# Kernel tuning notes

Measured on AMD Instinct MI355X. Metric: run time of the kernel, lower is better.

The kernel has to match this reference:

```python
import jax, jax.numpy as jnp
import numpy as np

KH, KW, PAD = 32, 32, 10  # kernel_size and padding from NeuralMem.__init__


def setup_inputs() -> dict:
    key = jax.random.key(0)
    k1, k2, k3, k4 = jax.random.split(key, 4)
    image = jax.random.normal(k1, (64, 64, 3), dtype=jnp.float32)
    mem = jax.random.normal(k2, (8192, 3072), dtype=jnp.float32)    # faiss IndexFlatL2 bank (keys)
    mem2 = jax.random.normal(k3, (8192, 3072), dtype=jnp.float32)   # faiss reconstruction bank (values)
    mapping = jax.random.randint(k4, (8192,), 0, 8192)              # Counter.most_common(1) vote table
    return {"image": image, "mem": mem, "mem2": mem2, "mapping": mapping}


def reference(image, mem, mem2, mapping):
    H, W, C = image.shape
    x = image.transpose(2, 0, 1)                       # [C,H,W]  (permute(2,0,1))
    xp = jnp.pad(x, ((0, 0), (PAD, PAD), (PAD, PAD)))  # unfold padding
    Lh = H + 2 * PAD - KH + 1
    Lw = W + 2 * PAD - KW + 1
    ii = jnp.arange(Lh)[:, None] + jnp.arange(KH)[None, :]  # [Lh,KH]
    jj = jnp.arange(Lw)[:, None] + jnp.arange(KW)[None, :]  # [Lw,KW]
    # unfold: patches [C,Lh,KH,Lw,KW] -> [L, C*KH*KW] with torch's (C,kh,kw) column order
    patches = xp[:, ii[:, :, None, None], jj[None, None, :, :]]
    patches = patches.transpose(1, 3, 0, 2, 4).reshape(Lh * Lw, C * KH * KW)  # [L,D]
    # L2 kNN (k=1): argmin ||p - m||^2 = argmin (||m||^2 - 2 p.m); ||p||^2 is constant per row
    mem_sq = jnp.sum(mem * mem, axis=1)                # [N]
    scores = patches @ mem.T                           # [L,N]
    nn = jnp.argmin(mem_sq[None, :] - 2.0 * scores, axis=1)  # [L]
    # counter majority vote -> mem2 reconstruct
    recon = mem2[mapping[nn]]                          # [L,D]
    # fold (sum of overlapping patches), then crop padding
    rp = recon.reshape(Lh, Lw, C, KH, KW).transpose(2, 0, 3, 1, 4)  # [C,Lh,KH,Lw,KW]
    outp = jnp.zeros_like(xp).at[:, ii[:, :, None, None], jj[None, None, :, :]].add(rp)
    out = outp[:, PAD:PAD + H, PAD:PAD + W]            # [C,H,W]
    out = out / jnp.max(out)                           # out / out.flatten().max()
    return out.transpose(1, 2, 0)                      # [H,W,C]
```

## Files before the change

### kernel.cpp

```cpp
#include <hip/hip_runtime.h>

typedef unsigned short u16;
typedef unsigned int   u32;
typedef int      i32x4  __attribute__((ext_vector_type(4)));
typedef float    f32x4  __attribute__((ext_vector_type(4)));
typedef _Float16 f16x8  __attribute__((ext_vector_type(8)));

#define LHW   53
#define NP    2809
#define KDIM  3072
#define NMEM  8192
#define PADW  84
#define IMG   64
#define MPAD  2816
#define BIGF  3.402823466e+38f
#define MARGIN 24.0f
#define QS    31.75f
#define C2    (2.0f / (QS * QS))

#define O_XP    0UL
#define O_MSQ   84736UL
#define O_MI8   117504UL
#define O_AI8   25283328UL
#define O_D     33934080UL
#define O_PVAL  80071424UL
#define O_ROWI  81524480UL
#define O_ACC   81535744UL
#define WS_NEED5 81584896UL

#define F_XP    0
#define F_MSQ   21504
#define F_PVAL  29696
#define F_PIDX  119584
#define F_ROW   209472
#define F_ACC   212288
#define F_MAX   224576
#define NSPL    32
#define NRANGE  (NMEM / NSPL)

__device__ inline char q8(float x) {
    float y = x * QS;
    y = fminf(fmaxf(y, -127.f), 127.f);
    return (char)__float2int_rn(y);
}

__global__ void k_xp(const float* __restrict__ image, float* __restrict__ xp,
                     float* __restrict__ accb) {
    int id = blockIdx.x * 256 + threadIdx.x;
    if (id < 12288) accb[id] = 0.f;
    if (id < 3 * PADW * PADW) {
        int c = id / (PADW * PADW), rem = id % (PADW * PADW);
        int py = rem / PADW, px = rem % PADW;
        float v = 0.f;
        if (py >= 10 && py < 74 && px >= 10 && px < 74)
            v = image[((py - 10) * IMG + (px - 10)) * 3 + c];
        xp[id] = v;
    }
}

__global__ __launch_bounds__(1024) void k_maxnorm(const float* __restrict__ acc,
                                                  float* __restrict__ out) {
    int t = threadIdx.x;
    float m = -BIGF;
    for (int i = t; i < 12288; i += 1024) m = fmaxf(m, acc[i]);
    #pragma unroll
    for (int s = 1; s < 64; s <<= 1) m = fmaxf(m, __shfl_xor(m, s));
    __shared__ float ls[16];
    int lane = t & 63, w = t >> 6;
    if (lane == 0) ls[w] = m;
    __syncthreads();
    float mv = ls[0];
    #pragma unroll
    for (int i = 1; i < 16; ++i) mv = fmaxf(mv, ls[i]);
    for (int i = t; i < 12288; i += 1024) {
        int c = i >> 12, y = (i >> 6) & 63, x = i & 63;
        out[(y * IMG + x) * 3 + c] = acc[i] / mv;
    }
}

__global__ __launch_bounds__(256) void k_quantmsq(const float* __restrict__ mem,
                                                  char* __restrict__ mq,
                                                  float* __restrict__ msq) {
    int j = blockIdx.x, t = threadIdx.x;
    const float4* r4 = (const float4*)(mem + (size_t)j * KDIM);
    char4* q4 = (char4*)(mq + (size_t)j * KDIM);
    float s = 0.f;
    #pragma unroll
    for (int i = 0; i < 3; ++i) {
        int idx = i * 256 + t;
        float4 v = r4[idx];
        s += v.x * v.x + v.y * v.y + v.z * v.z + v.w * v.w;
        char4 q = {q8(v.x), q8(v.y), q8(v.z), q8(v.w)};
        q4[idx] = q;
    }
    #pragma unroll
    for (int m = 1; m < 64; m <<= 1) s += __shfl_xor(s, m);
    __shared__ float ls[4];
    int lane = t & 63, w = t >> 6;
    if (lane == 0) ls[w] = s;
    __syncthreads();
    if (t == 0) msq[j] = ls[0] + ls[1] + ls[2] + ls[3];
}

__global__ __launch_bounds__(256) void k_quant_A(const float* __restrict__ xp,
                                                 char* __restrict__ aq) {
    int id = blockIdx.x * 256 + threadIdx.x;
    int e0 = id * 4;
    int p = e0 / KDIM, k = e0 - p * KDIM;
    char4 q = {0, 0, 0, 0};
    if (p < NP) {
        int c = k >> 10, kh = (k >> 5) & 31, kw = k & 31;
        int lh = p / LHW, lw = p - lh * LHW;
        const float* src = xp + c * (PADW * PADW) + (lh + kh) * PADW + lw + kw;
        q.x = q8(src[0]); q.y = q8(src[1]); q.z = q8(src[2]); q.w = q8(src[3]);
    }
    ((char4*)aq)[id] = q;
}

__global__ __launch_bounds__(256) void k_gemm_i8(
    const char* __restrict__ Aq, const char* __restrict__ Bq,
    const float* __restrict__ msq, _Float16* __restrict__ Dm,
    float* __restrict__ pval)
{
    __shared__ __align__(16) char lds[65536];
    const int t = threadIdx.x;
    const int lane = t & 63;
    const int w = t >> 6, wm = w >> 1, wn = w & 1;
    const int mrow = lane & 15;

    int L = blockIdx.x;
    int logical = (L & 7) * 176 + (L >> 3);
    int by = logical / 22, bx = logical - by * 22;
    const int rowBase = bx * 128;
    const int jBase   = by * 128;

    const int lrow = lane >> 3;
    const int gsrc = (lane & 7) ^ lrow;
    const char* gpl[8];
    unsigned ldsb[8];
    #pragma unroll
    for (int s = 0; s < 8; ++s) {
        int P = s >> 2, sub = s & 3;
        int row = sub * 32 + w * 8 + lrow;
        const char* basep = (P == 0 ? Aq : Bq);
        int gRow = (P == 0 ? rowBase : jBase) + row;
        gpl[s]  = basep + (size_t)gRow * KDIM + gsrc * 16;
        ldsb[s] = P * 16384 + (unsigned)(sub * 32 + w * 8) * 128;
    }

    i32x4 acc[4][4];
    #pragma unroll
    for (int i = 0; i < 4; ++i)
        #pragma unroll
        for (int j = 0; j < 4; ++j) { i32x4 z = {0, 0, 0, 0}; acc[i][j] = z; }

    #pragma unroll
    for (int s = 0; s < 8; ++s)
        __builtin_amdgcn_global_load_lds(
            (const __attribute__((address_space(1))) void*)(gpl[s]),
            (__attribute__((address_space(3))) void*)(lds + ldsb[s]),
            16, 0, 0);

    for (int kc = 0; kc < 24; ++kc) {
        const int cb = kc & 1;
        __syncthreads();
        if (kc < 23) {
            const unsigned nb = (cb ^ 1) * 32768u;
            #pragma unroll
            for (int s = 0; s < 8; ++s)
                __builtin_amdgcn_global_load_lds(
                    (const __attribute__((address_space(1))) void*)(gpl[s] + (kc + 1) * 128),
                    (__attribute__((address_space(3))) void*)(lds + nb + ldsb[s]),
                    16, 0, 0);
        }
        const char* lbase = lds + cb * 32768;
        #pragma unroll
        for (int kh2 = 0; kh2 < 2; ++kh2) {
            const int grp = kh2 * 4 + (lane >> 4);
            i32x4 ah[4];
            #pragma unroll
            for (int f = 0; f < 4; ++f) {
                int ra = wm * 64 + f * 16 + mrow;
                ah[f] = *(const i32x4*)(lbase + ra * 128 + (grp ^ (ra & 7)) * 16);
            }
            #pragma unroll
            for (int fj = 0; fj < 4; ++fj) {
                int rb = wn * 64 + fj * 16 + mrow;
                i32x4 bh = *(const i32x4*)(lbase + 16384 + rb * 128 + (grp ^ (rb & 7)) * 16);
                #pragma unroll
                for (int fi = 0; fi < 4; ++fi)
                    acc[fi][fj] = __builtin_amdgcn_mfma_i32_16x16x64_i8(ah[fi], bh, acc[fi][fj], 0, 0, 0);
            }
        }
    }

    float ms[4];
    #pragma unroll
    for (int fj = 0; fj < 4; ++fj) ms[fj] = msq[jBase + wn * 64 + fj * 16 + mrow] - 3072.0f;
    const int splitId = by * 2 + wn;
    #pragma unroll
    for (int fi = 0; fi < 4; ++fi) {
        #pragma unroll
        for (int r = 0; r < 4; ++r) {
            int p = rowBase + wm * 64 + fi * 16 + (lane >> 4) * 4 + r;
            float bv = BIGF;
            #pragma unroll
            for (int fj = 0; fj < 4; ++fj) {
                int j = jBase + wn * 64 + fj * 16 + mrow;
                float d = fmaf(-C2, (float)acc[fi][fj][r], ms[fj]);
                Dm[(size_t)p * NMEM + j] = (_Float16)d;
                bv = fminf(bv, d);
            }
            #pragma unroll
            for (int m = 1; m < 16; m <<= 1) bv = fminf(bv, __shfl_xor(bv, m));
            if (mrow == 0 && p < NP)
                pval[(size_t)p * 128 + splitId] = bv;
        }
    }
}

__global__ __launch_bounds__(256) void k_refine(
    const _Float16* __restrict__ Dm, const float* __restrict__ pval,
    const float* __restrict__ msq, const float* __restrict__ xp,
    const float* __restrict__ mem, const int* __restrict__ mapping,
    int* __restrict__ rowIdx)
{
    const int p = blockIdx.x, t = threadIdx.x;
    const _Float16* row = Dm + (size_t)p * NMEM;
    const int lane = t & 63, w = t >> 6;

    __shared__ float wred[4];
    __shared__ int lcnt;
    __shared__ int list[256];
    __shared__ float thr_s;

    float pm = (t < 128) ? pval[(size_t)p * 128 + t] : BIGF;
    #pragma unroll
    for (int m = 1; m < 64; m <<= 1) pm = fminf(pm, __shfl_xor(pm, m));
    if (lane == 0) wred[w] = pm;
    if (t == 0) lcnt = 0;
    __syncthreads();
    if (t == 0)
        thr_s = fminf(fminf(wred[0], wred[1]), fminf(wred[2], wred[3]))
                + (MARGIN + 0.5f);
    __syncthreads();
    const float th = thr_s;

    #pragma unroll
    for (int i0 = 0; i0 < 4; ++i0) {
        int base = i0 * 2048 + t * 8;
        f16x8 v = *(const f16x8*)(row + base);
        #pragma unroll
        for (int e = 0; e < 8; ++e)
            if ((float)v[e] <= th) {
                int sl = atomicAdd(&lcnt, 1);
                if (sl < 256) list[sl] = base + e;
            }
    }
    __syncthreads();
    int nc = min(lcnt, 256);

    const int lh = p / LHW, lw = p - (p / LHW) * LHW;
    float bd = BIGF; int bj = 0x7fffffff;
    __shared__ float tot;
    for (int ci = 0; ci < nc; ++ci) {
        int j = list[ci];
        const float* mrow2 = mem + (size_t)j * KDIM;
        float s = 0.f;
        for (int k = t; k < KDIM; k += 256) {
            int c = k >> 10, kh = (k >> 5) & 31, kw = k & 31;
            s += xp[c * (PADW * PADW) + (lh + kh) * PADW + lw + kw] * mrow2[k];
        }
        #pragma unroll
        for (int m = 1; m < 64; m <<= 1) s += __shfl_xor(s, m);
        if (lane == 0) wred[w] = s;
        __syncthreads();
        if (t == 0) tot = wred[0] + wred[1] + wred[2] + wred[3];
        __syncthreads();
        float d = msq[j] - 2.f * tot;
        if (d < bd || (d == bd && j < bj)) { bd = d; bj = j; }
    }
    if (t == 0) rowIdx[p] = mapping[bj];
}

#define LWCH 4
__global__ __launch_bounds__(256) void k_scatter(const float* __restrict__ mem2,
                                                 const int* __restrict__ rowIdx,
                                                 float* __restrict__ accb) {
    int b = blockIdx.x;
    int ch = b & (LWCH - 1);
    int lc = b >> 2;
    const int lh = lc / 3, c = lc % 3;
    const int lw0 = ch * 14, lw1 = min(53, lw0 + 14);
    __shared__ int r2s[53];
    const int t = threadIdx.x;
    if (t >= lw0 && t < lw1) r2s[t] = rowIdx[lh * LHW + t];
    __syncthreads();
    const int kh = t >> 3;
    const int g  = t & 7;
    float s[11];
    #pragma unroll
    for (int u = 0; u < 11; ++u) s[u] = 0.f;
    for (int lw = lw0; lw < lw1; ++lw) {
        const float* rowp = mem2 + (size_t)r2s[lw] * KDIM + c * 1024 + kh * 32;
        #pragma unroll
        for (int u = 0; u < 11; ++u) {
            int kw = g + 8 * u - lw;
            if (kw >= 0 && kw < 32) s[u] += rowp[kw];
        }
    }
    const int y = lh + kh - 10;
    if (y >= 0 && y < 64) {
        #pragma unroll
        for (int u = 0; u < 11; ++u) {
            int x = g + 8 * u - 10;
            if (x >= 0 && x < 64 && s[u] != 0.f)
                atomicAdd(&accb[c * 4096 + y * 64 + x], s[u]);
        }
    }
}

__global__ __launch_bounds__(256) void k_msq(const float* __restrict__ mem,
                                             float* __restrict__ msq) {
    int j = blockIdx.x;
    const float* row = mem + (size_t)j * KDIM;
    float s = 0.f;
    for (int i = threadIdx.x; i < KDIM; i += 256) { float v = row[i]; s += v * v; }
    #pragma unroll
    for (int m = 1; m < 64; m <<= 1) s += __shfl_xor(s, m);
    __shared__ float ls[4];
    int lane = threadIdx.x & 63, w = threadIdx.x >> 6;
    if (lane == 0) ls[w] = s;
    __syncthreads();
    if (threadIdx.x == 0) msq[j] = ls[0] + ls[1] + ls[2] + ls[3];
}

__global__ void k_amin(const float* __restrict__ pval, const int* __restrict__ pidx,
                       const int* __restrict__ mapping, int* __restrict__ rowIdx,
                       int nspl) {
    int p = blockIdx.x * 256 + threadIdx.x;
    if (p < NP) {
        float bv = BIGF; int bi = 0x7fffffff;
        for (int ns = 0; ns < nspl; ++ns) {
            float v = pval[(size_t)p * nspl + ns];
            int ix = pidx[(size_t)p * nspl + ns];
            if (v < bv || (v == bv && ix < bi)) { bv = v; bi = ix; }
        }
        rowIdx[p] = mapping[bi];
    }
}

__global__ __launch_bounds__(256) void k_gather(const float* __restrict__ mem2,
                                                const int* __restrict__ rowIdx,
                                                float* __restrict__ acc) {
    int b = blockIdx.x;
    int c = b >> 12, y = (b >> 6) & 63, x = b & 63;
    int khmin = max(0, y - 42), khmax = min(31, y + 10);
    int kwmin = max(0, x - 42), kwmax = min(31, x + 10);
    int nh = khmax - khmin + 1, nw = kwmax - kwmin + 1;
    int total = nh * nw;
    float s = 0.f;
    for (int idx = threadIdx.x; idx < total; idx += 256) {
        int kh = khmin + idx / nw;
        int kw = kwmin + idx % nw;
        int lh = y + 10 - kh, lw = x + 10 - kw;
        int p = lh * LHW + lw;
        int r2 = rowIdx[p];
        s += mem2[(size_t)r2 * KDIM + c * 1024 + kh * 32 + kw];
    }
    #pragma unroll
    for (int m = 1; m < 64; m <<= 1) s += __shfl_xor(s, m);
    __shared__ float ls[4];
    int lane = threadIdx.x & 63, w = threadIdx.x >> 6;
    if (lane == 0) ls[w] = s;
    __syncthreads();
    if (threadIdx.x == 0) acc[b] = ls[0] + ls[1] + ls[2] + ls[3];
}

__global__ __launch_bounds__(256) void k_gemm_argmin(
    const float* __restrict__ xp, const float* __restrict__ mem,
    const float* __restrict__ msq, float* __restrict__ pval,
    int* __restrict__ pidx)
{
    __shared__ float At[64][33];
    __shared__ float Bt[64][33];
    const int t = threadIdx.x;
    const int tx = t & 15, ty = t >> 4;
    const int rowBase = blockIdx.x * 64;
    const int nBase = blockIdx.y * NRANGE;

    float best[4]; int bidx[4];
    #pragma unroll
    for (int i = 0; i < 4; ++i) { best[i] = BIGF; bidx[i] = 0x7fffffff; }

    for (int nt = 0; nt < NRANGE / 64; ++nt) {
        const int jBase = nBase + nt * 64;
        float acc[4][4];
        #pragma unroll
        for (int i = 0; i < 4; ++i)
            #pragma unroll
            for (int j = 0; j < 4; ++j) acc[i][j] = 0.f;

        for (int kc = 0; kc < KDIM / 32; ++kc) {
            const int c = kc >> 5, kh = kc & 31;
            const float* xpc = xp + c * (PADW * PADW) + kh * PADW;
            #pragma unroll
            for (int i = 0; i < 8; ++i) {
                int e = i * 256 + t;
                int r = e >> 5, kwi = e & 31;
                int p = rowBase + r;
                float v = 0.f;
                if (p < NP) {
                    int lh = p / LHW, lw = p - lh * LHW;
                    v = xpc[lh * PADW + lw + kwi];
                }
                At[r][kwi] = v;
            }
            const float* mb = mem + (size_t)jBase * KDIM + kc * 32;
            #pragma unroll
            for (int i = 0; i < 8; ++i) {
                int e = i * 256 + t;
                int r = e >> 5, kwi = e & 31;
                Bt[r][kwi] = mb[(size_t)r * KDIM + kwi];
            }
            __syncthreads();
            #pragma unroll
            for (int kk = 0; kk < 32; ++kk) {
                float a[4], b[4];
                #pragma unroll
                for (int i = 0; i < 4; ++i) a[i] = At[ty + 16 * i][kk];
                #pragma unroll
                for (int j = 0; j < 4; ++j) b[j] = Bt[tx + 16 * j][kk];
                #pragma unroll
                for (int i = 0; i < 4; ++i)
                    #pragma unroll
                    for (int j = 0; j < 4; ++j) acc[i][j] += a[i] * b[j];
            }
            __syncthreads();
        }
        #pragma unroll
        for (int j = 0; j < 4; ++j) {
            int col = jBase + tx + 16 * j;
            float msv = msq[col];
            #pragma unroll
            for (int i = 0; i < 4; ++i) {
                float d = msv - 2.f * acc[i][j];
                if (d < best[i] || (d == best[i] && col < bidx[i])) {
                    best[i] = d; bidx[i] = col;
                }
            }
        }
    }
    #pragma unroll
    for (int m = 1; m < 16; m <<= 1) {
        #pragma unroll
        for (int i = 0; i < 4; ++i) {
            float ov = __shfl_xor(best[i], m);
            int   oi = __shfl_xor(bidx[i], m);
            if (ov < best[i] || (ov == best[i] && oi < bidx[i])) {
                best[i] = ov; bidx[i] = oi;
            }
        }
    }
    if (tx == 0) {
        #pragma unroll
        for (int i = 0; i < 4; ++i) {
            int p = rowBase + ty + 16 * i;
            if (p < NP) {
                pval[p * NSPL + blockIdx.y] = best[i];
                pidx[p * NSPL + blockIdx.y] = bidx[i];
            }
        }
    }
}

__global__ __launch_bounds__(256) void k_max(const float* __restrict__ acc,
                                             float* __restrict__ maxv) {
    float m = -BIGF;
    for (int i = threadIdx.x; i < 12288; i += 256) m = fmaxf(m, acc[i]);
    #pragma unroll
    for (int s = 1; s < 64; s <<= 1) m = fmaxf(m, __shfl_xor(m, s));
    __shared__ float ls[4];
    int lane = threadIdx.x & 63, w = threadIdx.x >> 6;
    if (lane == 0) ls[w] = m;
    __syncthreads();
    if (threadIdx.x == 0)
        maxv[0] = fmaxf(fmaxf(ls[0], ls[1]), fmaxf(ls[2], ls[3]));
}

__global__ void k_norm(const float* __restrict__ acc, const float* __restrict__ maxv,
                       float* __restrict__ out) {
    int id = blockIdx.x * 256 + threadIdx.x;
    if (id < 12288) {
        int c = id >> 12, y = (id >> 6) & 63, x = id & 63;
        out[(y * IMG + x) * 3 + c] = acc[id] / maxv[0];
    }
}

extern "C" void kernel_launch(void* const* d_in, const int* in_sizes, int n_in,
                              void* d_out, int out_size, void* d_ws, size_t ws_size,
                              hipStream_t stream) {
    const float* image   = (const float*)d_in[0];
    const float* mem     = (const float*)d_in[1];
    const float* mem2    = (const float*)d_in[2];
    const int*   mapping = (const int*)d_in[3];

    if (ws_size >= WS_NEED5) {
        char* wsB = (char*)d_ws;
        float*    xp   = (float*)(wsB + O_XP);
        float*    msq  = (float*)(wsB + O_MSQ);
        char*     mI8  = (char*)(wsB + O_MI8);
        char*     aI8  = (char*)(wsB + O_AI8);
        _Float16* Dm   = (_Float16*)(wsB + O_D);
        float*    pval = (float*)(wsB + O_PVAL);
        int*      rowI = (int*)(wsB + O_ROWI);
        float*    accb = (float*)(wsB + O_ACC);

        k_xp<<<dim3((3 * PADW * PADW + 255) / 256), 256, 0, stream>>>(image, xp, accb);
        k_quantmsq<<<dim3(NMEM), 256, 0, stream>>>(mem, mI8, msq);
        k_quant_A<<<dim3(MPAD * KDIM / 4 / 256), 256, 0, stream>>>(xp, aI8);
        k_gemm_i8<<<dim3(1408), 256, 0, stream>>>(aI8, mI8, msq, Dm, pval);
        k_refine<<<dim3(NP), 256, 0, stream>>>(Dm, pval, msq, xp, mem, mapping, rowI);
        k_scatter<<<dim3(LHW * 3 * LWCH), 256, 0, stream>>>(mem2, rowI, accb);
        k_maxnorm<<<dim3(1), 1024, 0, stream>>>(accb, (float*)d_out);
    } else {
        float* ws   = (float*)d_ws;
        float* xp   = ws + F_XP;
        float* msq  = ws + F_MSQ;
        float* pval = ws + F_PVAL;
        int*   pidx = (int*)(ws + F_PIDX);
        int*   rowI = (int*)(ws + F_ROW);
        float* acc  = ws + F_ACC;
        float* maxv = ws + F_MAX;

        k_xp<<<dim3((3 * PADW * PADW + 255) / 256), 256, 0, stream>>>(image, xp, acc);
        k_msq<<<dim3(NMEM), 256, 0, stream>>>(mem, msq);
        k_gemm_argmin<<<dim3((NP + 63) / 64, NSPL), 256, 0, stream>>>(xp, mem, msq, pval, pidx);
        k_amin<<<dim3((NP + 255) / 256), 256, 0, stream>>>(pval, pidx, mapping, rowI, NSPL);
        k_gather<<<dim3(3 * IMG * IMG), 256, 0, stream>>>(mem2, rowI, acc);
        k_max<<<dim3(1), 256, 0, stream>>>(acc, maxv);
        k_norm<<<dim3((12288 + 255) / 256), 256, 0, stream>>>(acc, maxv, (float*)d_out);
    }
}
```

Measured before the change: 202.2 us.

## Switch coarse kNN screening GEMM from int8 to FP4 scaled MFMA

Quantizes both the memory bank and the image patches to packed 4-bit E2M1 values instead of int8. The screening GEMM then uses the scaled f8f6f4 MFMA in FP4 mode, which halves the bytes loaded per row and the number of K iterations. The goal is to cut the cost of the coarse distance GEMM and of the quantization passes. Because FP4 is much coarser, the refine threshold margin grows from 24 to 128. That admits more candidates into exact refinement and risks dropping the true nearest neighbour if more than the capped 256 candidates fall inside the threshold.

```diff
diff --git a/kernel.cpp b/kernel.cpp
--- a/kernel.cpp
+++ b/kernel.cpp
@@ -3,6 +3,7 @@
 typedef unsigned short u16;
 typedef unsigned int   u32;
 typedef int      i32x4  __attribute__((ext_vector_type(4)));
+typedef int      i32x8  __attribute__((ext_vector_type(8)));
 typedef float    f32x4  __attribute__((ext_vector_type(4)));
 typedef _Float16 f16x8  __attribute__((ext_vector_type(8)));
 
@@ -14,19 +15,18 @@
 #define IMG   64
 #define MPAD  2816
 #define BIGF  3.402823466e+38f
-#define MARGIN 24.0f
-#define QS    31.75f
-#define C2    (2.0f / (QS * QS))
+#define MARGIN 128.0f
+#define ROWB  1536
 
 #define O_XP    0UL
 #define O_MSQ   84736UL
-#define O_MI8   117504UL
-#define O_AI8   25283328UL
-#define O_D     33934080UL
-#define O_PVAL  80071424UL
-#define O_ROWI  81524480UL
-#define O_ACC   81535744UL
-#define WS_NEED5 81584896UL
+#define O_MQ4   117504UL
+#define O_AQ4   12700416UL
+#define O_D     17025792UL
+#define O_PVAL  63163136UL
+#define O_ROWI  64604928UL
+#define O_ACC   64616192UL
+#define WS_NEED6 64665344UL
 
 #define F_XP    0
 #define F_MSQ   21504
@@ -38,10 +38,20 @@
 #define NSPL    32
 #define NRANGE  (NMEM / NSPL)
 
-__device__ inline char q8(float x) {
-    float y = x * QS;
-    y = fminf(fmaxf(y, -127.f), 127.f);
-    return (char)__float2int_rn(y);
+__device__ inline u32 q4(float x) {
+    float a = fminf(fabsf(x), 6.0f);
+    u32 s = (__float_as_uint(x) >> 31) << 3;
+    int v2;
+    if (a < 2.0f)      v2 = __float2int_rn(a * 2.0f);
+    else if (a < 4.0f) v2 = __float2int_rn(a) * 2;
+    else               v2 = __float2int_rn(a * 0.5f) * 4;
+    u32 e;
+    if (v2 <= 3)      e = (u32)v2;
+    else if (v2 == 4) e = 4u;
+    else if (v2 == 6) e = 5u;
+    else if (v2 == 8) e = 6u;
+    else              e = 7u;
+    return s | e;
 }
 
 __global__ void k_xp(const float* __restrict__ image, float* __restrict__ xp,
@@ -78,20 +88,19 @@
     }
 }
 
-__global__ __launch_bounds__(256) void k_quantmsq(const float* __restrict__ mem,
-                                                  char* __restrict__ mq,
-                                                  float* __restrict__ msq) {
+__global__ __launch_bounds__(256) void k_quantmsq4(const float* __restrict__ mem,
+                                                   u16* __restrict__ mq,
+                                                   float* __restrict__ msq) {
     int j = blockIdx.x, t = threadIdx.x;
-    const float4* r4 = (const float4*)(mem + (size_t)j * KDIM);
-    char4* q4 = (char4*)(mq + (size_t)j * KDIM);
+    const float4* r4 = (const float4*)(mem + (size_t)j * KDIM + t * 12);
+    u16* dst = mq + (size_t)j * (ROWB / 2) + t * 3;
     float s = 0.f;
     #pragma unroll
-    for (int i = 0; i < 3; ++i) {
-        int idx = i * 256 + t;
-        float4 v = r4[idx];
+    for (int g = 0; g < 3; ++g) {
+        float4 v = r4[g];
         s += v.x * v.x + v.y * v.y + v.z * v.z + v.w * v.w;
-        char4 q = {q8(v.x), q8(v.y), q8(v.z), q8(v.w)};
-        q4[idx] = q;
+        u32 pk = q4(v.x) | (q4(v.y) << 4) | (q4(v.z) << 8) | (q4(v.w) << 12);
+        dst[g] = (u16)pk;
     }
     #pragma unroll
     for (int m = 1; m < 64; m <<= 1) s += __shfl_xor(s, m);
@@ -102,22 +111,22 @@
     if (t == 0) msq[j] = ls[0] + ls[1] + ls[2] + ls[3];
 }
 
-__global__ __launch_bounds__(256) void k_quant_A(const float* __restrict__ xp,
-                                                 char* __restrict__ aq) {
+__global__ __launch_bounds__(256) void k_quantA4(const float* __restrict__ xp,
+                                                 u32* __restrict__ aq) {
     int id = blockIdx.x * 256 + threadIdx.x;
-    int e0 = id * 4;
-    int p = e0 / KDIM, k = e0 - p * KDIM;
-    char4 q = {0, 0, 0, 0};
+    int p = id / 384, k0 = (id - p * 384) * 8;
+    u32 pk = 0;
     if (p < NP) {
-        int c = k >> 10, kh = (k >> 5) & 31, kw = k & 31;
+        int c = k0 >> 10, kh = (k0 >> 5) & 31, kw = k0 & 31;
         int lh = p / LHW, lw = p - lh * LHW;
         const float* src = xp + c * (PADW * PADW) + (lh + kh) * PADW + lw + kw;
-        q.x = q8(src[0]); q.y = q8(src[1]); q.z = q8(src[2]); q.w = q8(src[3]);
-    }
-    ((char4*)aq)[id] = q;
-}
-
-__global__ __launch_bounds__(256) void k_gemm_i8(
+        #pragma unroll
+        for (int e = 0; e < 8; ++e) pk |= q4(src[e]) << (e * 4);
+    }
+    aq[id] = pk;
+}
+
+__global__ __launch_bounds__(256) void k_gemm_fp4(
     const char* __restrict__ Aq, const char* __restrict__ Bq,
     const float* __restrict__ msq, _Float16* __restrict__ Dm,
     float* __restrict__ pval)
@@ -144,15 +153,15 @@
         int row = sub * 32 + w * 8 + lrow;
         const char* basep = (P == 0 ? Aq : Bq);
         int gRow = (P == 0 ? rowBase : jBase) + row;
-        gpl[s]  = basep + (size_t)gRow * KDIM + gsrc * 16;
+        gpl[s]  = basep + (size_t)gRow * ROWB + gsrc * 16;
         ldsb[s] = P * 16384 + (unsigned)(sub * 32 + w * 8) * 128;
     }
 
-    i32x4 acc[4][4];
+    f32x4 acc[4][4];
     #pragma unroll
     for (int i = 0; i < 4; ++i)
         #pragma unroll
-        for (int j = 0; j < 4; ++j) { i32x4 z = {0, 0, 0, 0}; acc[i][j] = z; }
+        for (int j = 0; j < 4; ++j) { f32x4 z = {0.f, 0.f, 0.f, 0.f}; acc[i][j] = z; }
 
     #pragma unroll
     for (int s = 0; s < 8; ++s)
@@ -161,10 +170,10 @@
             (__attribute__((address_space(3))) void*)(lds + ldsb[s]),
             16, 0, 0);
 
-    for (int kc = 0; kc < 24; ++kc) {
+    for (int kc = 0; kc < 12; ++kc) {
         const int cb = kc & 1;
         __syncthreads();
-        if (kc < 23) {
+        if (kc < 11) {
             const unsigned nb = (cb ^ 1) * 32768u;
             #pragma unroll
             for (int s = 0; s < 8; ++s)
@@ -177,19 +186,24 @@
         #pragma unroll
         for (int kh2 = 0; kh2 < 2; ++kh2) {
             const int grp = kh2 * 4 + (lane >> 4);
-            i32x4 ah[4];
+            i32x8 ah[4];
             #pragma unroll
             for (int f = 0; f < 4; ++f) {
                 int ra = wm * 64 + f * 16 + mrow;
-                ah[f] = *(const i32x4*)(lbase + ra * 128 + (grp ^ (ra & 7)) * 16);
+                i32x4 d = *(const i32x4*)(lbase + ra * 128 + (grp ^ (ra & 7)) * 16);
+                i32x8 a8 = {d[0], d[1], d[2], d[3], d[0], d[1], d[2], d[3]};
+                ah[f] = a8;
             }
             #pragma unroll
             for (int fj = 0; fj < 4; ++fj) {
                 int rb = wn * 64 + fj * 16 + mrow;
-                i32x4 bh = *(const i32x4*)(lbase + 16384 + rb * 128 + (grp ^ (rb & 7)) * 16);
+                i32x4 db = *(const i32x4*)(lbase + 16384 + rb * 128 + (grp ^ (rb & 7)) * 16);
+                i32x8 bh = {db[0], db[1], db[2], db[3], db[0], db[1], db[2], db[3]};
                 #pragma unroll
                 for (int fi = 0; fi < 4; ++fi)
-                    acc[fi][fj] = __builtin_amdgcn_mfma_i32_16x16x64_i8(ah[fi], bh, acc[fi][fj], 0, 0, 0);
+                    acc[fi][fj] = __builtin_amdgcn_mfma_scale_f32_16x16x128_f8f6f4(
+                        ah[fi], bh, acc[fi][fj], 4, 4,
+                        0, 0x7F7F7F7F, 0, 0x7F7F7F7F);
             }
         }
     }
@@ -207,7 +221,7 @@
             #pragma unroll
             for (int fj = 0; fj < 4; ++fj) {
                 int j = jBase + wn * 64 + fj * 16 + mrow;
-                float d = fmaf(-C2, (float)acc[fi][fj][r], ms[fj]);
+                float d = fmaf(-2.0f, acc[fi][fj][r], ms[fj]);
                 Dm[(size_t)p * NMEM + j] = (_Float16)d;
                 bv = fminf(bv, d);
             }
@@ -242,7 +256,7 @@
     __syncthreads();
     if (t == 0)
         thr_s = fminf(fminf(wred[0], wred[1]), fminf(wred[2], wred[3]))
-                + (MARGIN + 0.5f);
+                + (MARGIN + 2.0f);
     __syncthreads();
     const float th = thr_s;
 
@@ -505,21 +519,22 @@
     const float* mem2    = (const float*)d_in[2];
     const int*   mapping = (const int*)d_in[3];
 
-    if (ws_size >= WS_NEED5) {
+    if (ws_size >= WS_NEED6) {
         char* wsB = (char*)d_ws;
         float*    xp   = (float*)(wsB + O_XP);
         float*    msq  = (float*)(wsB + O_MSQ);
-        char*     mI8  = (char*)(wsB + O_MI8);
-        char*     aI8  = (char*)(wsB + O_AI8);
+        u16*      mQ4  = (u16*)(wsB + O_MQ4);
+        u32*      aQ4  = (u32*)(wsB + O_AQ4);
         _Float16* Dm   = (_Float16*)(wsB + O_D);
         float*    pval = (float*)(wsB + O_PVAL);
         int*      rowI = (int*)(wsB + O_ROWI);
         float*    accb = (float*)(wsB + O_ACC);
 
         k_xp<<<dim3((3 * PADW * PADW + 255) / 256), 256, 0, stream>>>(image, xp, accb);
-        k_quantmsq<<<dim3(NMEM), 256, 0, stream>>>(mem, mI8, msq);
-        k_quant_A<<<dim3(MPAD * KDIM / 4 / 256), 256, 0, stream>>>(xp, aI8);
-        k_gemm_i8<<<dim3(1408), 256, 0, stream>>>(aI8, mI8, msq, Dm, pval);
+        k_quantmsq4<<<dim3(NMEM), 256, 0, stream>>>(mem, mQ4, msq);
+        k_quantA4<<<dim3(MPAD * 384 / 256), 256, 0, stream>>>(xp, aQ4);
+        k_gemm_fp4<<<dim3(1408), 256, 0, stream>>>((const char*)aQ4, (const char*)mQ4,
+                                                   msq, Dm, pval);
         k_refine<<<dim3(NP), 256, 0, stream>>>(Dm, pval, msq, xp, mem, mapping, rowI);
         k_scatter<<<dim3(LHW * 3 * LWCH), 256, 0, stream>>>(mem2, rowI, accb);
         k_maxnorm<<<dim3(1), 1024, 0, stream>>>(accb, (float*)d_out);
```

Measured after the change: 758.9 us. 3.75x slower.
